# Performance work log

Measured on AMD Instinct MI355X. Metric: run time of the kernel, lower is better.

Reference implementation:

```python
import jax, jax.numpy as jnp
import numpy as np

N_BUF = 60000.0
S_INIT = 2.0
S_INV = N_BUF ** S_INIT          # buffer init: N**S_init
S_HAT = (N_BUF ** 2) / S_INV     # == 1.0 at init


def setup_inputs() -> dict:
    key = jax.random.key(0)
    k1, k2 = jax.random.split(key)
    feats = jax.random.normal(k1, (16384, 128), dtype=jnp.float32)
    idx = jax.random.randint(k2, (16384,), 0, 60000).astype(jnp.int64)
    return {"feats": feats, "idx": idx}


def reference(feats, idx):
    # CauchyLoss.forward, faithful to the torch source. Note: the original
    # uses out-of-place masked_fill whose result is discarded, so neither the
    # diagonal nor the positive pairs are zeroed before the row-sum; we
    # replicate that exactly.
    n = feats.shape[0]
    B = n // 2
    sq = jnp.sum(feats * feats, axis=1)                      # [2B]
    d2 = sq[:, None] + sq[None, :] - 2.0 * (feats @ feats.T)  # [2B, 2B]
    d2 = jnp.maximum(d2, 0.0)
    q = 1.0 / (d2 + 1.0)                                      # [2B, 2B]
    # positive pairs: pos_mask = roll(eye(2B), B, dims=1) -> (i, (i+B) % 2B)
    rows = jnp.arange(n)
    qii = q[rows, (rows + B) % n]                             # [2B]
    attractive = -jnp.log(qii)
    repulsive = jnp.log(jnp.sum(q, axis=1)) * S_HAT           # [2B]
    return attractive.mean() + repulsive.mean()
```

## Files before the change

kernel.cpp:

```cpp
#include <hip/hip_runtime.h>
#include <hip/hip_bf16.h>

#define N 16384
#define D 128
#define NTI 128
#define GBLK2 4224
#define B_HALF 8192
#define PANEL 16384

typedef __attribute__((ext_vector_type(4))) float f32x4;

__device__ inline unsigned short f2bf(float x) {
    union { float f; unsigned u; } c; c.f = x;
    unsigned r = c.u + 0x7fffu + ((c.u >> 16) & 1u);
    return (unsigned short)(r >> 16);
}

__global__ __launch_bounds__(256)
void prep_kernel(const float* __restrict__ feats, unsigned char* __restrict__ fb8,
                 float* __restrict__ sq, float* __restrict__ rsum,
                 float* __restrict__ qii) {
    const int g  = blockIdx.x * 256 + threadIdx.x;
    const int p  = g >> 3;
    const int t8 = g & 7;
    const int i0 = p, i1 = p + B_HALF;
    const float4* ra = reinterpret_cast<const float4*>(feats + (size_t)i0 * D + t8 * 16);
    const float4* rb = reinterpret_cast<const float4*>(feats + (size_t)i1 * D + t8 * 16);
    char* da = (char*)fb8 + (size_t)(i0 >> 7) * PANEL + (size_t)(i0 & 127) * 8;
    char* db = (char*)fb8 + (size_t)(i1 >> 7) * PANEL + (size_t)(i1 & 127) * 8;
    float sa = 0.f, sb = 0.f, dot = 0.f;
#pragma unroll
    for (int c = 0; c < 2; ++c) {
        float4 x0 = ra[2 * c], x1 = ra[2 * c + 1];
        float4 y0 = rb[2 * c], y1 = rb[2 * c + 1];
        sa  += x0.x * x0.x + x0.y * x0.y + x0.z * x0.z + x0.w * x0.w
             + x1.x * x1.x + x1.y * x1.y + x1.z * x1.z + x1.w * x1.w;
        sb  += y0.x * y0.x + y0.y * y0.y + y0.z * y0.z + y0.w * y0.w
             + y1.x * y1.x + y1.y * y1.y + y1.z * y1.z + y1.w * y1.w;
        dot += x0.x * y0.x + x0.y * y0.y + x0.z * y0.z + x0.w * y0.w
             + x1.x * y1.x + x1.y * y1.y + x1.z * y1.z + x1.w * y1.w;
        int alo = __builtin_amdgcn_cvt_pk_fp8_f32(x0.x, x0.y, 0, 0);
        alo     = __builtin_amdgcn_cvt_pk_fp8_f32(x0.z, x0.w, alo, 1);
        int ahi = __builtin_amdgcn_cvt_pk_fp8_f32(x1.x, x1.y, 0, 0);
        ahi     = __builtin_amdgcn_cvt_pk_fp8_f32(x1.z, x1.w, ahi, 1);
        int blo = __builtin_amdgcn_cvt_pk_fp8_f32(y0.x, y0.y, 0, 0);
        blo     = __builtin_amdgcn_cvt_pk_fp8_f32(y0.z, y0.w, blo, 1);
        int bhi = __builtin_amdgcn_cvt_pk_fp8_f32(y1.x, y1.y, 0, 0);
        bhi     = __builtin_amdgcn_cvt_pk_fp8_f32(y1.z, y1.w, bhi, 1);
        const int ks = 2 * t8 + c;
        *reinterpret_cast<int2*>(da + ks * 1024) = make_int2(alo, ahi);
        *reinterpret_cast<int2*>(db + ks * 1024) = make_int2(blo, bhi);
    }
    sa  += __shfl_xor(sa, 1);  sa  += __shfl_xor(sa, 2);  sa  += __shfl_xor(sa, 4);
    sb  += __shfl_xor(sb, 1);  sb  += __shfl_xor(sb, 2);  sb  += __shfl_xor(sb, 4);
    dot += __shfl_xor(dot, 1); dot += __shfl_xor(dot, 2); dot += __shfl_xor(dot, 4);
    if (t8 == 0) {
        sq[i0] = sa; sq[i1] = sb;
        rsum[i0] = 0.f; rsum[i1] = 0.f;
        float d2 = fmaxf(sa + sb - 2.f * dot, 0.f);
        float q = 1.f / (d2 + 1.f);
        qii[i0] = q; qii[i1] = q;
    }
}

__global__ __launch_bounds__(256, 5)
void gram_kernel(const unsigned char* __restrict__ fb8, const float* __restrict__ sq,
                 float* __restrict__ rsum) {
    const int bid  = (blockIdx.x & 7) * (GBLK2 / 8) + (blockIdx.x >> 3);
    const int chnk = bid >> 1;
    const int half = bid & 1;

    int u = (int)((130.0f - sqrtf(16900.0f - 8.0f * (float)chnk)) * 0.25f);
    if (u < 0) u = 0; if (u > 31) u = 31;
    while (u > 0 && 2 * u * (65 - u) > chnk) --u;
    while (2 * (u + 1) * (64 - u) <= chnk) ++u;
    int rem = chnk - 2 * u * (65 - u);
    const int cnt = 32 - u;
    int sub = 0;
    while (rem >= cnt) { rem -= cnt; ++sub; }
    const int ti  = 4 * u + sub;
    const int tj0 = ti + 4 * rem;
    const int nt  = (NTI - tj0 < 4) ? (NTI - tj0) : 4;

    const int lane = threadIdx.x & 63;
    const int wid  = threadIdx.x >> 6;
    const int wr   = wid >> 1;
    const int wc   = wid & 1;
    const int lrow = lane & 15;
    const int lk   = lane >> 4;
    const int row0 = half * 64 + wr * 32;

    const char* pa = (const char*)fb8 + (size_t)ti * PANEL;
    const int aoff0 = lk * 1024 + (row0 + lrow) * 8;
    const int boff0 = lk * 1024 + (wc * 64 + lrow) * 8;

    long avh[4][2];
#pragma unroll
    for (int kk = 0; kk < 4; ++kk)
#pragma unroll
        for (int m = 0; m < 2; ++m)
            avh[kk][m] = *reinterpret_cast<const long*>(pa + aoff0 + kk * 4096 + m * 128);

    float SA[2][4];
#pragma unroll
    for (int m = 0; m < 2; ++m) {
        const float4 v = *reinterpret_cast<const float4*>(
            sq + ti * 128 + row0 + m * 16 + lk * 4);
        SA[m][0] = -0.5f * v.x; SA[m][1] = -0.5f * v.y;
        SA[m][2] = -0.5f * v.z; SA[m][3] = -0.5f * v.w;
    }
    float SB[4][4];
#pragma unroll
    for (int t = 0; t < 4; ++t) {
        const int tt = (tj0 + t < NTI) ? (tj0 + t) : (NTI - 1);
#pragma unroll
        for (int n = 0; n < 4; ++n)
            SB[t][n] = -0.5f * (sq[tt * 128 + wc * 64 + n * 16 + lrow] + 1.0f);
    }

    float racc[2][4];
#pragma unroll
    for (int m = 0; m < 2; ++m)
#pragma unroll
        for (int r = 0; r < 4; ++r) racc[m][r] = 0.f;

#pragma unroll
    for (int t = 0; t < 4; ++t) {
        if (t < nt) {
            const char* pb = (const char*)fb8 + (size_t)(tj0 + t) * PANEL;

            f32x4 acc[2][4];
#pragma unroll
            for (int m = 0; m < 2; ++m)
#pragma unroll
                for (int n = 0; n < 4; ++n)
#pragma unroll
                    for (int r = 0; r < 4; ++r)
                        acc[m][n][r] = SA[m][r] + SB[t][n];

#pragma unroll
            for (int kk = 0; kk < 4; ++kk) {
                long bv[4];
#pragma unroll
                for (int n = 0; n < 4; ++n)
                    bv[n] = *reinterpret_cast<const long*>(pb + boff0 + kk * 4096 + n * 128);
#pragma unroll
                for (int m = 0; m < 2; ++m)
#pragma unroll
                    for (int n = 0; n < 4; ++n)
                        acc[m][n] = __builtin_amdgcn_mfma_f32_16x16x32_fp8_fp8(
                            avh[kk][m], bv[n], acc[m][n], 0, 0, 0);
            }

            float cloc[4] = {0.f, 0.f, 0.f, 0.f};
#pragma unroll
            for (int m = 0; m < 2; ++m)
#pragma unroll
                for (int n = 0; n < 4; ++n)
#pragma unroll
                    for (int r = 0; r < 4; ++r) {
                        float a = fminf(acc[m][n][r], -0.5f);
                        float q = __builtin_amdgcn_rcpf(a);
                        racc[m][r] += q;
                        cloc[n] += q;
                    }
            if (tj0 + t != ti) {
#pragma unroll
                for (int n = 0; n < 4; ++n) {
                    float v = cloc[n];
                    v += __shfl_xor(v, 16);
                    v += __shfl_xor(v, 32);
                    if (lane < 16)
                        atomicAdd(&rsum[(tj0 + t) * 128 + wc * 64 + n * 16 + lrow],
                                  -0.5f * v);
                }
            }
        }
    }

#pragma unroll
    for (int m = 0; m < 2; ++m)
#pragma unroll
        for (int r = 0; r < 4; ++r) {
            float v = racc[m][r];
            v += __shfl_xor(v, 1);
            v += __shfl_xor(v, 2);
            v += __shfl_xor(v, 4);
            v += __shfl_xor(v, 8);
            if (lrow == 0)
                atomicAdd(&rsum[ti * 128 + row0 + m * 16 + lk * 4 + r], -0.5f * v);
        }
}

__global__ __launch_bounds__(256)
void finish1_kernel(const float* __restrict__ rsum, const float* __restrict__ qii,
                    float* __restrict__ partial) {
    __shared__ float red[4];
    const int i = blockIdx.x * 256 + threadIdx.x;
    float v = __logf(rsum[i]) - __logf(qii[i]);
#pragma unroll
    for (int m = 32; m >= 1; m >>= 1) v += __shfl_xor(v, m);
    if ((threadIdx.x & 63) == 0) red[threadIdx.x >> 6] = v;
    __syncthreads();
    if (threadIdx.x == 0) partial[blockIdx.x] = red[0] + red[1] + red[2] + red[3];
}

__global__ __launch_bounds__(64)
void finish2_kernel(const float* __restrict__ partial, unsigned* __restrict__ out) {
    float v = partial[threadIdx.x];
#pragma unroll
    for (int m = 32; m >= 1; m >>= 1) v += __shfl_xor(v, m);
    if (threadIdx.x == 0) {
        float val = v / (float)N;
        union { float f; unsigned u; } c; c.f = val;
        out[0] = (c.u & 0xFFFF0000u) | (unsigned)f2bf(val);
    }
}

extern "C" void kernel_launch(void* const* d_in, const int* in_sizes, int n_in,
                              void* d_out, int out_size, void* d_ws, size_t ws_size,
                              hipStream_t stream) {
    const float* feats = (const float*)d_in[0];
    char* ws = (char*)d_ws;
    unsigned char* fb8 = (unsigned char*)ws;
    float* sq      = (float*)(ws + (size_t)N * D);
    float* rsum    = (float*)(ws + (size_t)N * D + (size_t)N * 4);
    float* qii     = (float*)(ws + (size_t)N * D + (size_t)N * 8);
    float* partial = (float*)(ws + (size_t)N * D + (size_t)N * 12);

    hipLaunchKernelGGL(prep_kernel, dim3(256), dim3(256), 0, stream,
                       feats, fb8, sq, rsum, qii);
    hipLaunchKernelGGL(gram_kernel, dim3(GBLK2), dim3(256), 0, stream,
                       fb8, sq, rsum);
    hipLaunchKernelGGL(finish1_kernel, dim3(64), dim3(256), 0, stream,
                       rsum, qii, partial);
    hipLaunchKernelGGL(finish2_kernel, dim3(1), dim3(64), 0, stream,
                       partial, (unsigned*)d_out);
}
```

Measured before the change: 86.32 us.

## Use 16x16x128 scaled FP8 MFMA with row-major panel layout and quarter-tile blocks

Replaces the four 16x16x32 FP8 MFMAs per output tile with a single gfx950 scaled 16x16x128 f8f6f4 MFMA that uses unit scales. The FP8 panel layout changes from k-sliced to row-major 128 bytes per row, so each lane loads 32 contiguous bytes. Each block now covers a 32-row quarter tile instead of a half tile, which doubles the grid and lowers the occupancy hint from 5 to 3. The intent is fewer MFMA issues and wider loads, at the cost of more blocks, more duplicated B-panel loads and more column atomics.

```diff
diff --git a/kernel.cpp b/kernel.cpp
--- a/kernel.cpp
+++ b/kernel.cpp
@@ -4,16 +4,27 @@
 #define N 16384
 #define D 128
 #define NTI 128
-#define GBLK2 4224
+#define GBLK3 8448
 #define B_HALF 8192
 #define PANEL 16384
 
+typedef __attribute__((ext_vector_type(8))) int   i32x8;
+typedef __attribute__((ext_vector_type(4))) int   i32x4;
 typedef __attribute__((ext_vector_type(4))) float f32x4;
 
 __device__ inline unsigned short f2bf(float x) {
     union { float f; unsigned u; } c; c.f = x;
     unsigned r = c.u + 0x7fffu + ((c.u >> 16) & 1u);
     return (unsigned short)(r >> 16);
+}
+
+__device__ __forceinline__ i32x8 ld32(const char* p) {
+    i32x4 lo = *reinterpret_cast<const i32x4*>(p);
+    i32x4 hi = *reinterpret_cast<const i32x4*>(p + 16);
+    i32x8 v;
+    v[0] = lo[0]; v[1] = lo[1]; v[2] = lo[2]; v[3] = lo[3];
+    v[4] = hi[0]; v[5] = hi[1]; v[6] = hi[2]; v[7] = hi[3];
+    return v;
 }
 
 __global__ __launch_bounds__(256)
@@ -26,8 +37,8 @@
     const int i0 = p, i1 = p + B_HALF;
     const float4* ra = reinterpret_cast<const float4*>(feats + (size_t)i0 * D + t8 * 16);
     const float4* rb = reinterpret_cast<const float4*>(feats + (size_t)i1 * D + t8 * 16);
-    char* da = (char*)fb8 + (size_t)(i0 >> 7) * PANEL + (size_t)(i0 & 127) * 8;
-    char* db = (char*)fb8 + (size_t)(i1 >> 7) * PANEL + (size_t)(i1 & 127) * 8;
+    char* da = (char*)fb8 + (size_t)(i0 >> 7) * PANEL + (size_t)(i0 & 127) * 128;
+    char* db = (char*)fb8 + (size_t)(i1 >> 7) * PANEL + (size_t)(i1 & 127) * 128;
     float sa = 0.f, sb = 0.f, dot = 0.f;
 #pragma unroll
     for (int c = 0; c < 2; ++c) {
@@ -48,8 +59,9 @@
         int bhi = __builtin_amdgcn_cvt_pk_fp8_f32(y1.x, y1.y, 0, 0);
         bhi     = __builtin_amdgcn_cvt_pk_fp8_f32(y1.z, y1.w, bhi, 1);
         const int ks = 2 * t8 + c;
-        *reinterpret_cast<int2*>(da + ks * 1024) = make_int2(alo, ahi);
-        *reinterpret_cast<int2*>(db + ks * 1024) = make_int2(blo, bhi);
+        const int poff = (ks & 3) * 32 + (ks >> 2) * 8;
+        *reinterpret_cast<int2*>(da + poff) = make_int2(alo, ahi);
+        *reinterpret_cast<int2*>(db + poff) = make_int2(blo, bhi);
     }
     sa  += __shfl_xor(sa, 1);  sa  += __shfl_xor(sa, 2);  sa  += __shfl_xor(sa, 4);
     sb  += __shfl_xor(sb, 1);  sb  += __shfl_xor(sb, 2);  sb  += __shfl_xor(sb, 4);
@@ -63,12 +75,12 @@
     }
 }
 
-__global__ __launch_bounds__(256, 5)
+__global__ __launch_bounds__(256, 3)
 void gram_kernel(const unsigned char* __restrict__ fb8, const float* __restrict__ sq,
                  float* __restrict__ rsum) {
-    const int bid  = (blockIdx.x & 7) * (GBLK2 / 8) + (blockIdx.x >> 3);
-    const int chnk = bid >> 1;
-    const int half = bid & 1;
+    const int bid  = (blockIdx.x & 7) * (GBLK3 / 8) + (blockIdx.x >> 3);
+    const int chnk = bid >> 2;
+    const int quar = bid & 3;
 
     int u = (int)((130.0f - sqrtf(16900.0f - 8.0f * (float)chnk)) * 0.25f);
     if (u < 0) u = 0; if (u > 31) u = 31;
@@ -88,108 +100,83 @@
     const int wc   = wid & 1;
     const int lrow = lane & 15;
     const int lk   = lane >> 4;
-    const int row0 = half * 64 + wr * 32;
+    const int row0 = quar * 32 + wr * 16;
 
     const char* pa = (const char*)fb8 + (size_t)ti * PANEL;
-    const int aoff0 = lk * 1024 + (row0 + lrow) * 8;
-    const int boff0 = lk * 1024 + (wc * 64 + lrow) * 8;
-
-    long avh[4][2];
-#pragma unroll
-    for (int kk = 0; kk < 4; ++kk)
-#pragma unroll
-        for (int m = 0; m < 2; ++m)
-            avh[kk][m] = *reinterpret_cast<const long*>(pa + aoff0 + kk * 4096 + m * 128);
-
-    float SA[2][4];
-#pragma unroll
-    for (int m = 0; m < 2; ++m) {
+
+    const i32x8 av = ld32(pa + (row0 + lrow) * 128 + lk * 32);
+
+    float SA[4];
+    {
         const float4 v = *reinterpret_cast<const float4*>(
-            sq + ti * 128 + row0 + m * 16 + lk * 4);
-        SA[m][0] = -0.5f * v.x; SA[m][1] = -0.5f * v.y;
-        SA[m][2] = -0.5f * v.z; SA[m][3] = -0.5f * v.w;
-    }
-    float SB[4][4];
-#pragma unroll
-    for (int t = 0; t < 4; ++t) {
-        const int tt = (tj0 + t < NTI) ? (tj0 + t) : (NTI - 1);
-#pragma unroll
-        for (int n = 0; n < 4; ++n)
-            SB[t][n] = -0.5f * (sq[tt * 128 + wc * 64 + n * 16 + lrow] + 1.0f);
-    }
-
-    float racc[2][4];
-#pragma unroll
-    for (int m = 0; m < 2; ++m)
-#pragma unroll
-        for (int r = 0; r < 4; ++r) racc[m][r] = 0.f;
+            sq + ti * 128 + row0 + lk * 4);
+        SA[0] = -0.5f * v.x; SA[1] = -0.5f * v.y;
+        SA[2] = -0.5f * v.z; SA[3] = -0.5f * v.w;
+    }
+
+    float racc[4] = {0.f, 0.f, 0.f, 0.f};
 
 #pragma unroll
     for (int t = 0; t < 4; ++t) {
         if (t < nt) {
-            const char* pb = (const char*)fb8 + (size_t)(tj0 + t) * PANEL;
-
-            f32x4 acc[2][4];
-#pragma unroll
-            for (int m = 0; m < 2; ++m)
-#pragma unroll
-                for (int n = 0; n < 4; ++n)
-#pragma unroll
-                    for (int r = 0; r < 4; ++r)
-                        acc[m][n][r] = SA[m][r] + SB[t][n];
-
-#pragma unroll
-            for (int kk = 0; kk < 4; ++kk) {
-                long bv[4];
-#pragma unroll
-                for (int n = 0; n < 4; ++n)
-                    bv[n] = *reinterpret_cast<const long*>(pb + boff0 + kk * 4096 + n * 128);
-#pragma unroll
-                for (int m = 0; m < 2; ++m)
-#pragma unroll
-                    for (int n = 0; n < 4; ++n)
-                        acc[m][n] = __builtin_amdgcn_mfma_f32_16x16x32_fp8_fp8(
-                            avh[kk][m], bv[n], acc[m][n], 0, 0, 0);
-            }
-
-            float cloc[4] = {0.f, 0.f, 0.f, 0.f};
-#pragma unroll
-            for (int m = 0; m < 2; ++m)
-#pragma unroll
-                for (int n = 0; n < 4; ++n)
-#pragma unroll
-                    for (int r = 0; r < 4; ++r) {
-                        float a = fminf(acc[m][n][r], -0.5f);
-                        float q = __builtin_amdgcn_rcpf(a);
-                        racc[m][r] += q;
-                        cloc[n] += q;
-                    }
-            if (tj0 + t != ti) {
-#pragma unroll
-                for (int n = 0; n < 4; ++n) {
-                    float v = cloc[n];
-                    v += __shfl_xor(v, 16);
-                    v += __shfl_xor(v, 32);
+            const int tt = tj0 + t;
+            const char* pb = (const char*)fb8 + (size_t)tt * PANEL;
+
+            float SBn[4];
+#pragma unroll
+            for (int n = 0; n < 4; ++n)
+                SBn[n] = -0.5f * (sq[tt * 128 + wc * 64 + n * 16 + lrow] + 1.0f);
+
+            i32x8 bv[4];
+#pragma unroll
+            for (int n = 0; n < 4; ++n)
+                bv[n] = ld32(pb + (wc * 64 + n * 16 + lrow) * 128 + lk * 32);
+
+            f32x4 acc[4];
+#pragma unroll
+            for (int n = 0; n < 4; ++n)
+#pragma unroll
+                for (int r = 0; r < 4; ++r)
+                    acc[n][r] = SA[r] + SBn[n];
+
+#pragma unroll
+            for (int n = 0; n < 4; ++n)
+                acc[n] = __builtin_amdgcn_mfma_scale_f32_16x16x128_f8f6f4(
+                    av, bv[n], acc[n], 0 , 0 ,
+                    0, 0x7F7F7F7F ,
+                    0, 0x7F7F7F7F );
+
+#pragma unroll
+            for (int n = 0; n < 4; ++n) {
+                float cloc = 0.f;
+#pragma unroll
+                for (int r = 0; r < 4; ++r) {
+                    float a = fminf(acc[n][r], -0.5f);
+                    float q = __builtin_amdgcn_rcpf(a);
+                    racc[r] += q;
+                    cloc += q;
+                }
+                if (tt != ti) {
+                    cloc += __shfl_xor(cloc, 16);
+                    cloc += __shfl_xor(cloc, 32);
                     if (lane < 16)
-                        atomicAdd(&rsum[(tj0 + t) * 128 + wc * 64 + n * 16 + lrow],
-                                  -0.5f * v);
+                        atomicAdd(&rsum[tt * 128 + wc * 64 + n * 16 + lrow],
+                                  -0.5f * cloc);
                 }
             }
         }
     }
 
 #pragma unroll
-    for (int m = 0; m < 2; ++m)
-#pragma unroll
-        for (int r = 0; r < 4; ++r) {
-            float v = racc[m][r];
-            v += __shfl_xor(v, 1);
-            v += __shfl_xor(v, 2);
-            v += __shfl_xor(v, 4);
-            v += __shfl_xor(v, 8);
-            if (lrow == 0)
-                atomicAdd(&rsum[ti * 128 + row0 + m * 16 + lk * 4 + r], -0.5f * v);
-        }
+    for (int r = 0; r < 4; ++r) {
+        float v = racc[r];
+        v += __shfl_xor(v, 1);
+        v += __shfl_xor(v, 2);
+        v += __shfl_xor(v, 4);
+        v += __shfl_xor(v, 8);
+        if (lrow == 0)
+            atomicAdd(&rsum[ti * 128 + row0 + lk * 4 + r], -0.5f * v);
+    }
 }
 
 __global__ __launch_bounds__(256)
@@ -230,7 +217,7 @@
 
     hipLaunchKernelGGL(prep_kernel, dim3(256), dim3(256), 0, stream,
                        feats, fb8, sq, rsum, qii);
-    hipLaunchKernelGGL(gram_kernel, dim3(GBLK2), dim3(256), 0, stream,
+    hipLaunchKernelGGL(gram_kernel, dim3(GBLK3), dim3(256), 0, stream,
                        fb8, sq, rsum);
     hipLaunchKernelGGL(finish1_kernel, dim3(64), dim3(256), 0, stream,
                        rsum, qii, partial);
```

After: 147.3 us. +70.6%, slower.
